# Performance work log

Hardware: AMD Instinct MI355X
Metric: run time of the kernel (lower is better)

The kernel has to match this reference:

```python
import jax, jax.numpy as jnp
import numpy as np

U = 356  # LSTM units

def _lstm(x, W, Wr, b, h0, c0):
    """Keras-style LSTM. x: [B,T,F]. Returns (hs [B,T,U], h [B,U], c [B,U])."""
    def step(carry, xt):
        h, c = carry
        z = xt @ W + h @ Wr + b            # [B, 4U], gate order i,f,g,o
        i, f, g, o = jnp.split(z, 4, axis=-1)
        c = jax.nn.sigmoid(f) * c + jax.nn.sigmoid(i) * jnp.tanh(g)
        h = jax.nn.sigmoid(o) * jnp.tanh(c)
        return (h, c), h
    (h, c), hs = jax.lax.scan(step, (h0, c0), jnp.swapaxes(x, 0, 1))
    return jnp.swapaxes(hs, 0, 1), h, c


def setup_inputs() -> dict:
    key = jax.random.key(0)
    ks = jax.random.split(key, 12)
    s = 0.05
    return {
        "x": jax.random.normal(ks[0], (8192, 7, 69), jnp.float32),
        "m": jax.random.normal(ks[1], (8192, 7, 45), jnp.float32),
        "enc_W": jax.random.normal(ks[2], (69, 4 * U), jnp.float32) * s,
        "enc_U": jax.random.normal(ks[3], (U, 4 * U), jnp.float32) * s,
        "enc_b": jnp.zeros((4 * U,), jnp.float32),
        "dec_W": jax.random.normal(ks[4], (45, 4 * U), jnp.float32) * s,
        "dec_U": jax.random.normal(ks[5], (U, 4 * U), jnp.float32) * s,
        "dec_b": jnp.zeros((4 * U,), jnp.float32),
        "W_map": jax.random.normal(ks[6], (7 * U, 1024), jnp.float32) * s,
        "b_map": jnp.zeros((1024,), jnp.float32),
        "W1": jax.random.normal(ks[7], (1024, 1024), jnp.float32) * s,
        "b1": jnp.zeros((1024,), jnp.float32),
        "W2": jax.random.normal(ks[8], (1024, 1024), jnp.float32) * s,
        "b2": jnp.zeros((1024,), jnp.float32),
        "W3": jax.random.normal(ks[9], (1024, 1024), jnp.float32) * s,
        "b3": jnp.zeros((1024,), jnp.float32),
        "W_out": jax.random.normal(ks[10], (1024, 168), jnp.float32) * s,
        "b_out": jnp.zeros((168,), jnp.float32),
    }


def reference(x, m, enc_W, enc_U, enc_b, dec_W, dec_U, dec_b,
              W_map, b_map, W1, b1, W2, b2, W3, b3, W_out, b_out):
    B = x.shape[0]
    h0 = jnp.zeros((B, U), x.dtype)
    c0 = jnp.zeros((B, U), x.dtype)
    # Encoder: only final states are used (dropout layers are identity at inference).
    _, s_h, s_c = _lstm(x, enc_W, enc_U, enc_b, h0, c0)
    # Decoder seeded with encoder states, returns full sequence [B,7,U].
    decoded, _, _ = _lstm(m, dec_W, dec_U, dec_b, s_h, s_c)
    f = decoded.reshape(B, -1)                     # [B, 7*356]
    h = jax.nn.relu(f @ W_map + b_map)
    h = jnp.tanh(h @ W1 + b1)
    h = jnp.tanh(h @ W2 + b2)
    h = jnp.tanh(h @ W3 + b3)
    return h @ W_out + b_out                        # [B, 168]
```

## Files before the change

kernel.cpp:

```cpp
#include <hip/hip_runtime.h>
#include <math.h>


using bf16x8 = __attribute__((ext_vector_type(8))) short;
using f32x4  = __attribute__((ext_vector_type(4))) float;

enum { EPI_NONE = 0, EPI_RELU = 1, EPI_TANH = 2 };

__device__ inline unsigned short f2bf(float f) {
    union { float f; unsigned u; } v; v.f = f;
    unsigned r = v.u + 0x7FFFu + ((v.u >> 16) & 1u);
    return (unsigned short)(r >> 16);
}
__device__ inline float sigf(float x) {
    return __fdividef(1.f, 1.f + __expf(-x));
}
__device__ inline float tanhfast(float x) {
    return 1.f - __fdividef(2.f, 1.f + __expf(2.f * x));
}

__device__ inline void gll16(const void* g, void* l) {
    __builtin_amdgcn_global_load_lds(
        (const __attribute__((address_space(1))) unsigned int*)(uintptr_t)g,
        (__attribute__((address_space(3))) unsigned int*)(unsigned int)(uintptr_t)l,
        16, 0, 0);
}

#define STAGE(A_, Bt_, K_, k0_, b_)                                            \
    {                                                                          \
        const int row = tid >> 2, kc = tid & 3;                                \
        gll16((A_)  + (size_t)(m0 + row) * (K_) + (k0_) + kc * 8,              \
              (void*)&As[b_][tid * 8]);                                        \
        gll16((Bt_) + (size_t)(n0 + row) * (K_) + (k0_) + kc * 8,              \
              (void*)&Bs[b_][tid * 8]);                                        \
    }

#define GEMM_CORE(A_, Bt_, K_)                                                 \
    STAGE(A_, Bt_, K_, 0, 0)                                                   \
    {                                                                          \
        const int niter = (K_) / 32;                                           \
        for (int it = 0; it < niter; ++it) {                                   \
            __syncthreads();                                                   \
            if (it + 1 < niter) {                                              \
                const int kn = (it + 1) * 32, bn = (it + 1) & 1;               \
                STAGE(A_, Bt_, K_, kn, bn)                                     \
            }                                                                  \
            const unsigned short* Asb = As[it & 1];                            \
            const unsigned short* Bsb = Bs[it & 1];                            \
            bf16x8 aF[2], bF[4];                                               \
            _Pragma("unroll")                                                  \
            for (int mi = 0; mi < 2; ++mi)                                     \
                aF[mi] = *(const bf16x8*)(Asb + (wr*32 + mi*16 + lm)*32 + quad*8);\
            _Pragma("unroll")                                                  \
            for (int ni = 0; ni < 4; ++ni)                                     \
                bF[ni] = *(const bf16x8*)(Bsb + (wc*64 + ni*16 + lm)*32 + quad*8);\
            _Pragma("unroll")                                                  \
            for (int mi = 0; mi < 2; ++mi)                                     \
                _Pragma("unroll")                                              \
                for (int ni = 0; ni < 4; ++ni)                                 \
                    acc[mi][ni] = __builtin_amdgcn_mfma_f32_16x16x32_bf16(     \
                        aF[mi], bF[ni], acc[mi][ni], 0, 0, 0);                 \
        }                                                                      \
    }

#define GEMM_PREAMBLE                                                          \
    __shared__ __attribute__((aligned(16))) unsigned short As[2][128 * 32];    \
    __shared__ __attribute__((aligned(16))) unsigned short Bs[2][128 * 32];    \
    const int tid  = threadIdx.x;                                              \
    const int lane = tid & 63;                                                 \
    const int w    = tid >> 6;                                       \
    const int wr   = w >> 1, wc = w & 1;                    \
    const int lm   = lane & 15, quad = lane >> 4;                              \
    const int m0   = blockIdx.x * 128, n0 = blockIdx.y * 128;                  \
    f32x4 acc[2][4] = {};

template <int EPI, int OUT_BF16, int NGUARD>
__global__ __launch_bounds__(512, 6)
void gemm_mfma(const unsigned short* __restrict__ A,
               const unsigned short* __restrict__ Bt,
               const float* __restrict__ bias,
               void* __restrict__ Cv, int ldc, int Nreal, int K)
{
    GEMM_PREAMBLE
    GEMM_CORE(A, Bt, K)
    #pragma unroll
    for (int mi = 0; mi < 2; ++mi)
        #pragma unroll
        for (int r = 0; r < 4; ++r) {
            const size_t row = m0 + wr * 32 + mi * 16 + quad * 4 + r;
            #pragma unroll
            for (int ni = 0; ni < 4; ++ni) {
                const int col = n0 + wc * 64 + ni * 16 + lm;
                if (!NGUARD || col < Nreal) {
                    float v = acc[mi][ni][r] + bias[col];
                    if (EPI == EPI_RELU) v = fmaxf(v, 0.f);
                    if (EPI == EPI_TANH) v = tanhfast(v);
                    if (OUT_BF16) ((unsigned short*)Cv)[row * ldc + col] = f2bf(v);
                    else          ((float*)Cv)[row * ldc + col] = v;
                }
            }
        }
}

__global__ __launch_bounds__(512, 6)
void gemm_lstm(const unsigned short* __restrict__ A,
               const unsigned short* __restrict__ Bt,
               const float* __restrict__ biasI,
               float* __restrict__ c,
               unsigned short* __restrict__ hdst, int ldh, int hoff,
               unsigned short* __restrict__ dec, int doff, int K)
{
    GEMM_PREAMBLE
    GEMM_CORE(A, Bt, K)
    const int u = ((n0 + wc * 64) >> 6) * 16 + lm;
    if (u >= 356) return;
    float bI[4];
    #pragma unroll
    for (int ni = 0; ni < 4; ++ni) bI[ni] = biasI[n0 + wc * 64 + ni * 16 + lm];
    #pragma unroll
    for (int mi = 0; mi < 2; ++mi)
        #pragma unroll
        for (int r = 0; r < 4; ++r) {
            const size_t row = m0 + wr * 32 + mi * 16 + quad * 4 + r;
            const float zi = acc[mi][0][r] + bI[0];
            const float zf = acc[mi][1][r] + bI[1];
            const float zg = acc[mi][2][r] + bI[2];
            const float zo = acc[mi][3][r] + bI[3];
            const size_t ci = row * 356 + u;
            const float cn = sigf(zf) * c[ci] + sigf(zi) * tanhfast(zg);
            c[ci] = cn;
            const unsigned short hb = f2bf(sigf(zo) * tanhfast(cn));
            if (hdst) hdst[row * (size_t)ldh + hoff + u] = hb;
            if (dec)  dec[row * (size_t)2496 + doff + u] = hb;
        }
}

struct PackArgs {
    const float *Wa0, *Wb0, *bias0; unsigned short* Wt0; float* bI0; int K10, K0, Kp0;
    const float *Wa1, *Wb1, *bias1; unsigned short* Wt1; float* bI1; int K11, K1, Kp1;
};
__global__ void pack_lstm2(PackArgs p)
{
    const float* Wa  = blockIdx.y ? p.Wa1  : p.Wa0;
    const float* Wb  = blockIdx.y ? p.Wb1  : p.Wb0;
    const float* bias= blockIdx.y ? p.bias1: p.bias0;
    unsigned short* Wt = blockIdx.y ? p.Wt1 : p.Wt0;
    float* biasI = blockIdx.y ? p.bI1 : p.bI0;
    const int K1 = blockIdx.y ? p.K11 : p.K10;
    const int K  = blockIdx.y ? p.K1  : p.K0;
    const int Kp = blockIdx.y ? p.Kp1 : p.Kp0;
    const int idx = blockIdx.x * 256 + threadIdx.x;
    if (idx >= 1536 * Kp) return;
    const int np = idx / Kp, k = idx - np * Kp;
    const int ub = np >> 6, g = (np >> 4) & 3, ul = np & 15;
    const int u = ub * 16 + ul;
    const bool valid = (u < 356);
    const int norig = g * 356 + u;
    float v = 0.f;
    if (valid && k < K)
        v = (k < K1) ? Wa[(size_t)k * 1424 + norig]
                     : Wb[(size_t)(k - K1) * 1424 + norig];
    Wt[(size_t)np * Kp + k] = f2bf(v);
    if (k == 0) biasI[np] = valid ? bias[norig] : 0.f;
}

__global__ void transpose_pack(const float* __restrict__ W, int K, int N,
                               unsigned short* __restrict__ Wt, int Kp, int Np)
{
    __shared__ float t[32][33];
    const int n0 = blockIdx.x * 32, k0 = blockIdx.y * 32;
    const int tx = threadIdx.x, ty = threadIdx.y;
    #pragma unroll
    for (int r = 0; r < 4; ++r) {
        const int k = k0 + ty + 8 * r, n = n0 + tx;
        t[ty + 8 * r][tx] = (k < K && n < N) ? W[(size_t)k * N + n] : 0.f;
    }
    __syncthreads();
    #pragma unroll
    for (int r = 0; r < 4; ++r) {
        const int k = k0 + tx, n = n0 + ty + 8 * r;
        if (k < Kp && n < Np) Wt[(size_t)n * Kp + k] = f2bf(t[tx][ty + 8 * r]);
    }
}

struct WP3 { const float *s0, *s1, *s2; unsigned short *d0, *d1, *d2; };
__global__ void transpose_pack3(WP3 p)
{
    __shared__ float t[32][33];
    const float* W = (blockIdx.z == 0) ? p.s0 : (blockIdx.z == 1) ? p.s1 : p.s2;
    unsigned short* Wt = (blockIdx.z == 0) ? p.d0 : (blockIdx.z == 1) ? p.d1 : p.d2;
    const int n0 = blockIdx.x * 32, k0 = blockIdx.y * 32;
    const int tx = threadIdx.x, ty = threadIdx.y;
    #pragma unroll
    for (int r = 0; r < 4; ++r)
        t[ty + 8 * r][tx] = W[(size_t)(k0 + ty + 8 * r) * 1024 + n0 + tx];
    __syncthreads();
    #pragma unroll
    for (int r = 0; r < 4; ++r)
        Wt[(size_t)(n0 + ty + 8 * r) * 1024 + k0 + tx] = f2bf(t[tx][ty + 8 * r]);
}

__global__ void zero_pads(unsigned short* __restrict__ AcE,
                          unsigned short* __restrict__ AcD,
                          unsigned short* __restrict__ dcd,
                          unsigned short* __restrict__ cc)
{
    const size_t N0 = (size_t)8192 * 379, N1 = (size_t)6 * 8192 * 23;
    const size_t N2 = (size_t)8192 * 371, N3 = (size_t)6 * 8192 * 15;
    const size_t N4 = (size_t)8192 * 4,   N5 = (size_t)8192 * 356 * 2;
    size_t i = (size_t)blockIdx.x * 256 + threadIdx.x;
    if (i < N0) { const size_t r = i / 379; AcE[r * 448 + 69 + i % 379] = 0; return; }
    i -= N0;
    if (i < N1) { const size_t r = 8192 + i / 23; AcE[r * 448 + 425 + i % 23] = 0; return; }
    i -= N1;
    if (i < N2) { const size_t r = i / 371; AcD[r * 416 + 45 + i % 371] = 0; return; }
    i -= N2;
    if (i < N3) { const size_t r = 8192 + i / 15; AcD[r * 416 + 401 + i % 15] = 0; return; }
    i -= N3;
    if (i < N4) { dcd[(i / 4) * 2496 + 2492 + (i & 3)] = 0; return; }
    i -= N4;
    if (i < N5) cc[i] = 0;
}

__global__ void fill_slices2(const float* __restrict__ x,
                             const float* __restrict__ m,
                             unsigned short* __restrict__ AcE,
                             unsigned short* __restrict__ AcD)
{
    const int NX = 8192 * 7 * 69;
    int i = blockIdx.x * 256 + threadIdx.x;
    if (i < NX) {
        const int b = i / (7 * 69), rem = i - b * 7 * 69;
        const int t = rem / 69, f = rem - t * 69;
        AcE[(size_t)t * 8192 * 448 + (size_t)b * 448 + f] = f2bf(x[i]);
        return;
    }
    i -= NX;
    if (i < 8192 * 7 * 45) {
        const int b = i / (7 * 45), rem = i - b * 7 * 45;
        const int t = rem / 45, f = rem - t * 45;
        AcD[(size_t)t * 8192 * 416 + (size_t)b * 416 + f] = f2bf(m[i]);
    }
}

extern "C" void kernel_launch(void* const* d_in, const int* in_sizes, int n_in,
                              void* d_out, int out_size, void* d_ws, size_t ws_size,
                              hipStream_t stream)
{
    const float* x     = (const float*)d_in[0];
    const float* m     = (const float*)d_in[1];
    const float* enc_W = (const float*)d_in[2];
    const float* enc_U = (const float*)d_in[3];
    const float* enc_b = (const float*)d_in[4];
    const float* dec_W = (const float*)d_in[5];
    const float* dec_Um= (const float*)d_in[6];
    const float* dec_b = (const float*)d_in[7];
    const float* W_map = (const float*)d_in[8];
    const float* b_map = (const float*)d_in[9];
    const float* W1    = (const float*)d_in[10];
    const float* b1    = (const float*)d_in[11];
    const float* W2    = (const float*)d_in[12];
    const float* b2    = (const float*)d_in[13];
    const float* W3    = (const float*)d_in[14];
    const float* b3    = (const float*)d_in[15];
    const float* W_out = (const float*)d_in[16];
    const float* b_out = (const float*)d_in[17];
    float* out = (float*)d_out;

    const int B = 8192, T = 7, FE = 69, FD = 45;
    const int KE = 448, KD = 416, KMP = 2496;

    char* ws = (char*)d_ws;
    size_t off = 0;
    auto alloc = [&](size_t bytes) -> void* {
        void* p = ws + off; off = (off + bytes + 255) & ~(size_t)255; return p;
    };
    unsigned short* WtE = (unsigned short*)alloc((size_t)1536 * KE * 2);
    unsigned short* WtD = (unsigned short*)alloc((size_t)1536 * KD * 2);
    unsigned short* WtM = (unsigned short*)alloc((size_t)1024 * KMP * 2);
    unsigned short* Wt1 = (unsigned short*)alloc((size_t)1024 * 1024 * 2);
    unsigned short* Wt2 = (unsigned short*)alloc((size_t)1024 * 1024 * 2);
    unsigned short* Wt3 = (unsigned short*)alloc((size_t)1024 * 1024 * 2);
    unsigned short* WtO = (unsigned short*)alloc((size_t)256 * 1024 * 2);
    float* bIE = (float*)alloc(1536 * 4);
    float* bID = (float*)alloc(1536 * 4);
    unsigned short* AcE = (unsigned short*)alloc((size_t)T * B * KE * 2);
    unsigned short* AcD = (unsigned short*)alloc((size_t)T * B * KD * 2);
    unsigned short* dcd = (unsigned short*)alloc((size_t)B * KMP * 2);
    unsigned short* a1  = (unsigned short*)alloc((size_t)B * 1024 * 2);
    unsigned short* a2  = (unsigned short*)alloc((size_t)B * 1024 * 2);
    float* c = (float*)alloc((size_t)B * 356 * 4);

    PackArgs pa{enc_W, enc_U, enc_b, WtE, bIE, FE, FE + 356, KE,
                dec_W, dec_Um, dec_b, WtD, bID, FD, FD + 356, KD};
    pack_lstm2<<<dim3((1536 * KE + 255) / 256, 2), 256, 0, stream>>>(pa);
    const dim3 tb(32, 8);
    transpose_pack<<<dim3(1024 / 32, KMP / 32), tb, 0, stream>>>(
        W_map, 2492, 1024, WtM, KMP, 1024);
    WP3 p3{W1, W2, W3, Wt1, Wt2, Wt3};
    transpose_pack3<<<dim3(32, 32, 3), tb, 0, stream>>>(p3);
    transpose_pack<<<dim3(256 / 32, 1024 / 32), tb, 0, stream>>>(
        W_out, 1024, 168, WtO, 1024, 256);

    {
        const size_t tot = (size_t)8192 * 379 + (size_t)6 * 8192 * 23
                         + (size_t)8192 * 371 + (size_t)6 * 8192 * 15
                         + (size_t)8192 * 4   + (size_t)8192 * 356 * 2;
        zero_pads<<<(unsigned)((tot + 255) / 256), 256, 0, stream>>>(
            AcE, AcD, dcd, (unsigned short*)c);
    }
    fill_slices2<<<(B * T * (FE + FD) + 255) / 256, 256, 0, stream>>>(
        x, m, AcE, AcD);

    const dim3 gz(64, 12);
    for (int t = 0; t < T; ++t) {
        unsigned short* At = AcE + (size_t)t * B * KE;
        unsigned short* hdst = (t < 6) ? AcE + (size_t)(t + 1) * B * KE : AcD;
        gemm_lstm<<<gz, 512, 0, stream>>>(
            At, WtE, bIE, c, hdst, (t < 6) ? KE : KD, (t < 6) ? FE : FD,
            nullptr, 0, KE);
    }
    for (int t = 0; t < T; ++t) {
        unsigned short* At = AcD + (size_t)t * B * KD;
        unsigned short* hdst = (t < 6) ? AcD + (size_t)(t + 1) * B * KD : nullptr;
        gemm_lstm<<<gz, 512, 0, stream>>>(
            At, WtD, bID, c, hdst, KD, FD, dcd, t * 356, KD);
    }

    gemm_mfma<EPI_RELU, 1, 0><<<dim3(64, 8), 512, 0, stream>>>(
        dcd, WtM, b_map, a1, 1024, 1024, KMP);
    gemm_mfma<EPI_TANH, 1, 0><<<dim3(64, 8), 512, 0, stream>>>(
        a1, Wt1, b1, a2, 1024, 1024, 1024);
    gemm_mfma<EPI_TANH, 1, 0><<<dim3(64, 8), 512, 0, stream>>>(
        a2, Wt2, b2, a1, 1024, 1024, 1024);
    gemm_mfma<EPI_TANH, 1, 0><<<dim3(64, 8), 512, 0, stream>>>(
        a1, Wt3, b3, a2, 1024, 1024, 1024);
    gemm_mfma<EPI_NONE, 0, 1><<<dim3(64, 2), 512, 0, stream>>>(
        a2, WtO, b_out, out, 168, 168, 1024);
}
```

Before: 614.3 us.

## Fuse all 14 LSTM timesteps into one persistent kernel with on-chip state

Replaces the 14 per-timestep GEMM+cell launches, the padding-zero kernel and the input-slice fill kernel with a single persistent kernel. Each block owns 32 batch rows, keeps h in LDS and c in registers across all encoder and decoder steps, and converts x/m into LDS on the fly. Weights are streamed from global/L2 directly into registers each step. This removes launch overhead and the global round-trips for h, c and the staged inputs. In exchange, only 256 blocks run, each repeatedly rereading the full weight matrix without LDS staging, which may limit MFMA utilisation.

```diff
diff --git a/kernel.cpp b/kernel.cpp
--- a/kernel.cpp
+++ b/kernel.cpp
@@ -25,6 +25,121 @@
         (__attribute__((address_space(3))) unsigned int*)(unsigned int)(uintptr_t)l,
         16, 0, 0);
 }
+
+#define PROWS 32
+#define PLDA  456
+
+__global__ __launch_bounds__(512, 2)
+void lstm_persist(const float* __restrict__ x,
+                  const float* __restrict__ m,
+                  const unsigned short* __restrict__ WtE,
+                  const unsigned short* __restrict__ WtD,
+                  const float* __restrict__ bIE,
+                  const float* __restrict__ bID,
+                  unsigned short* __restrict__ dcd)
+{
+    __shared__ __attribute__((aligned(16))) unsigned short Ab[PROWS * PLDA];
+    const int tid  = threadIdx.x;
+    const int lane = tid & 63;
+    const int w    = tid >> 6;
+    const int lm   = lane & 15, quad = lane >> 4;
+    const int brow = blockIdx.x * PROWS;
+
+    for (int i = tid; i < PROWS * PLDA; i += 512) Ab[i] = 0;
+    __syncthreads();
+    for (int i = tid; i < PROWS * 69; i += 512) {
+        const int r = i / 69, f = i - r * 69;
+        Ab[r * PLDA + f] = f2bf(x[((size_t)(brow + r) * 7 + 0) * 69 + f]);
+    }
+
+    float creg[2][3][4] = {};
+    float bI[3][4];
+
+    for (int s = 0; s < 14; ++s) {
+        const bool enc = (s < 7);
+        const int t = enc ? s : s - 7;
+        const unsigned short* Wt = enc ? WtE : WtD;
+        const unsigned short* wbase =
+            Wt + (size_t)(w * 192 + lm) * 448 + quad * 8;
+
+        if (s == 0 || s == 7) {
+            const float* bsrc = enc ? bIE : bID;
+            #pragma unroll
+            for (int a = 0; a < 3; ++a)
+                #pragma unroll
+                for (int g = 0; g < 4; ++g)
+                    bI[a][g] = bsrc[(3 * w + a) * 64 + g * 16 + lm];
+        }
+
+        __syncthreads();
+
+        f32x4 acc[2][12] = {};
+        #pragma unroll 2
+        for (int kk = 0; kk < 14; ++kk) {
+            bf16x8 aF[2];
+            #pragma unroll
+            for (int mi = 0; mi < 2; ++mi)
+                aF[mi] = *(const bf16x8*)&Ab[(mi * 16 + lm) * PLDA
+                                             + kk * 32 + quad * 8];
+            bf16x8 bF[12];
+            #pragma unroll
+            for (int ni = 0; ni < 12; ++ni)
+                bF[ni] = *(const bf16x8*)(wbase + (size_t)ni * 16 * 448
+                                          + kk * 32);
+            #pragma unroll
+            for (int ni = 0; ni < 12; ++ni) {
+                acc[0][ni] = __builtin_amdgcn_mfma_f32_16x16x32_bf16(
+                    aF[0], bF[ni], acc[0][ni], 0, 0, 0);
+                acc[1][ni] = __builtin_amdgcn_mfma_f32_16x16x32_bf16(
+                    aF[1], bF[ni], acc[1][ni], 0, 0, 0);
+            }
+        }
+
+        __syncthreads();
+
+        const int hoff = (s < 6) ? 69 : 45;
+        #pragma unroll
+        for (int mi = 0; mi < 2; ++mi)
+            #pragma unroll
+            for (int a = 0; a < 3; ++a) {
+                const int u = (3 * w + a) * 16 + lm;
+                const bool uok = (u < 356);
+                #pragma unroll
+                for (int r = 0; r < 4; ++r) {
+                    const float zi = acc[mi][a * 4 + 0][r] + bI[a][0];
+                    const float zf = acc[mi][a * 4 + 1][r] + bI[a][1];
+                    const float zg = acc[mi][a * 4 + 2][r] + bI[a][2];
+                    const float zo = acc[mi][a * 4 + 3][r] + bI[a][3];
+                    const float cn = sigf(zf) * creg[mi][a][r]
+                                   + sigf(zi) * tanhfast(zg);
+                    creg[mi][a][r] = cn;
+                    const unsigned short hb = f2bf(sigf(zo) * tanhfast(cn));
+                    const int rl = mi * 16 + quad * 4 + r;
+                    if (uok) {
+                        if (s < 13) Ab[rl * PLDA + hoff + u] = hb;
+                        if (!enc)
+                            dcd[(size_t)(brow + rl) * 2496 + t * 356 + u] = hb;
+                    }
+                }
+            }
+
+        const int sn = s + 1;
+        if (sn < 7) {
+            for (int i = tid; i < PROWS * 69; i += 512) {
+                const int r = i / 69, f = i - r * 69;
+                Ab[r * PLDA + f] =
+                    f2bf(x[((size_t)(brow + r) * 7 + sn) * 69 + f]);
+            }
+        } else if (sn < 14) {
+            for (int i = tid; i < PROWS * 45; i += 512) {
+                const int r = i / 45, f = i - r * 45;
+                Ab[r * PLDA + f] =
+                    f2bf(m[((size_t)(brow + r) * 7 + (sn - 7)) * 45 + f]);
+            }
+        }
+    }
+}
+
 
 #define STAGE(A_, Bt_, K_, k0_, b_)                                            \
     {                                                                          \
@@ -102,39 +217,6 @@
         }
 }
 
-__global__ __launch_bounds__(512, 6)
-void gemm_lstm(const unsigned short* __restrict__ A,
-               const unsigned short* __restrict__ Bt,
-               const float* __restrict__ biasI,
-               float* __restrict__ c,
-               unsigned short* __restrict__ hdst, int ldh, int hoff,
-               unsigned short* __restrict__ dec, int doff, int K)
-{
-    GEMM_PREAMBLE
-    GEMM_CORE(A, Bt, K)
-    const int u = ((n0 + wc * 64) >> 6) * 16 + lm;
-    if (u >= 356) return;
-    float bI[4];
-    #pragma unroll
-    for (int ni = 0; ni < 4; ++ni) bI[ni] = biasI[n0 + wc * 64 + ni * 16 + lm];
-    #pragma unroll
-    for (int mi = 0; mi < 2; ++mi)
-        #pragma unroll
-        for (int r = 0; r < 4; ++r) {
-            const size_t row = m0 + wr * 32 + mi * 16 + quad * 4 + r;
-            const float zi = acc[mi][0][r] + bI[0];
-            const float zf = acc[mi][1][r] + bI[1];
-            const float zg = acc[mi][2][r] + bI[2];
-            const float zo = acc[mi][3][r] + bI[3];
-            const size_t ci = row * 356 + u;
-            const float cn = sigf(zf) * c[ci] + sigf(zi) * tanhfast(zg);
-            c[ci] = cn;
-            const unsigned short hb = f2bf(sigf(zo) * tanhfast(cn));
-            if (hdst) hdst[row * (size_t)ldh + hoff + u] = hb;
-            if (dec)  dec[row * (size_t)2496 + doff + u] = hb;
-        }
-}
-
 struct PackArgs {
     const float *Wa0, *Wb0, *bias0; unsigned short* Wt0; float* bI0; int K10, K0, Kp0;
     const float *Wa1, *Wb1, *bias1; unsigned short* Wt1; float* bI1; int K11, K1, Kp1;
@@ -200,47 +282,10 @@
         Wt[(size_t)(n0 + ty + 8 * r) * 1024 + k0 + tx] = f2bf(t[tx][ty + 8 * r]);
 }
 
-__global__ void zero_pads(unsigned short* __restrict__ AcE,
-                          unsigned short* __restrict__ AcD,
-                          unsigned short* __restrict__ dcd,
-                          unsigned short* __restrict__ cc)
-{
-    const size_t N0 = (size_t)8192 * 379, N1 = (size_t)6 * 8192 * 23;
-    const size_t N2 = (size_t)8192 * 371, N3 = (size_t)6 * 8192 * 15;
-    const size_t N4 = (size_t)8192 * 4,   N5 = (size_t)8192 * 356 * 2;
-    size_t i = (size_t)blockIdx.x * 256 + threadIdx.x;
-    if (i < N0) { const size_t r = i / 379; AcE[r * 448 + 69 + i % 379] = 0; return; }
-    i -= N0;
-    if (i < N1) { const size_t r = 8192 + i / 23; AcE[r * 448 + 425 + i % 23] = 0; return; }
-    i -= N1;
-    if (i < N2) { const size_t r = i / 371; AcD[r * 416 + 45 + i % 371] = 0; return; }
-    i -= N2;
-    if (i < N3) { const size_t r = 8192 + i / 15; AcD[r * 416 + 401 + i % 15] = 0; return; }
-    i -= N3;
-    if (i < N4) { dcd[(i / 4) * 2496 + 2492 + (i & 3)] = 0; return; }
-    i -= N4;
-    if (i < N5) cc[i] = 0;
-}
-
-__global__ void fill_slices2(const float* __restrict__ x,
-                             const float* __restrict__ m,
-                             unsigned short* __restrict__ AcE,
-                             unsigned short* __restrict__ AcD)
-{
-    const int NX = 8192 * 7 * 69;
-    int i = blockIdx.x * 256 + threadIdx.x;
-    if (i < NX) {
-        const int b = i / (7 * 69), rem = i - b * 7 * 69;
-        const int t = rem / 69, f = rem - t * 69;
-        AcE[(size_t)t * 8192 * 448 + (size_t)b * 448 + f] = f2bf(x[i]);
-        return;
-    }
-    i -= NX;
-    if (i < 8192 * 7 * 45) {
-        const int b = i / (7 * 45), rem = i - b * 7 * 45;
-        const int t = rem / 45, f = rem - t * 45;
-        AcD[(size_t)t * 8192 * 416 + (size_t)b * 416 + f] = f2bf(m[i]);
-    }
+__global__ void zero_dcd_pad(unsigned short* __restrict__ dcd)
+{
+    const int i = blockIdx.x * 256 + threadIdx.x;
+    if (i < 8192 * 4) dcd[(size_t)(i >> 2) * 2496 + 2492 + (i & 3)] = 0;
 }
 
 extern "C" void kernel_launch(void* const* d_in, const int* in_sizes, int n_in,
@@ -267,16 +312,16 @@
     const float* b_out = (const float*)d_in[17];
     float* out = (float*)d_out;
 
-    const int B = 8192, T = 7, FE = 69, FD = 45;
-    const int KE = 448, KD = 416, KMP = 2496;
+    const int B = 8192, FE = 69, FD = 45;
+    const int KMP = 2496;
 
     char* ws = (char*)d_ws;
     size_t off = 0;
     auto alloc = [&](size_t bytes) -> void* {
         void* p = ws + off; off = (off + bytes + 255) & ~(size_t)255; return p;
     };
-    unsigned short* WtE = (unsigned short*)alloc((size_t)1536 * KE * 2);
-    unsigned short* WtD = (unsigned short*)alloc((size_t)1536 * KD * 2);
+    unsigned short* WtE = (unsigned short*)alloc((size_t)1536 * 448 * 2);
+    unsigned short* WtD = (unsigned short*)alloc((size_t)1536 * 448 * 2);
     unsigned short* WtM = (unsigned short*)alloc((size_t)1024 * KMP * 2);
     unsigned short* Wt1 = (unsigned short*)alloc((size_t)1024 * 1024 * 2);
     unsigned short* Wt2 = (unsigned short*)alloc((size_t)1024 * 1024 * 2);
@@ -284,16 +329,13 @@
     unsigned short* WtO = (unsigned short*)alloc((size_t)256 * 1024 * 2);
     float* bIE = (float*)alloc(1536 * 4);
     float* bID = (float*)alloc(1536 * 4);
-    unsigned short* AcE = (unsigned short*)alloc((size_t)T * B * KE * 2);
-    unsigned short* AcD = (unsigned short*)alloc((size_t)T * B * KD * 2);
     unsigned short* dcd = (unsigned short*)alloc((size_t)B * KMP * 2);
     unsigned short* a1  = (unsigned short*)alloc((size_t)B * 1024 * 2);
     unsigned short* a2  = (unsigned short*)alloc((size_t)B * 1024 * 2);
-    float* c = (float*)alloc((size_t)B * 356 * 4);
-
-    PackArgs pa{enc_W, enc_U, enc_b, WtE, bIE, FE, FE + 356, KE,
-                dec_W, dec_Um, dec_b, WtD, bID, FD, FD + 356, KD};
-    pack_lstm2<<<dim3((1536 * KE + 255) / 256, 2), 256, 0, stream>>>(pa);
+
+    PackArgs pa{enc_W, enc_U, enc_b, WtE, bIE, FE, FE + 356, 448,
+                dec_W, dec_Um, dec_b, WtD, bID, FD, FD + 356, 448};
+    pack_lstm2<<<dim3((1536 * 448 + 255) / 256, 2), 256, 0, stream>>>(pa);
     const dim3 tb(32, 8);
     transpose_pack<<<dim3(1024 / 32, KMP / 32), tb, 0, stream>>>(
         W_map, 2492, 1024, WtM, KMP, 1024);
@@ -301,31 +343,9 @@
     transpose_pack3<<<dim3(32, 32, 3), tb, 0, stream>>>(p3);
     transpose_pack<<<dim3(256 / 32, 1024 / 32), tb, 0, stream>>>(
         W_out, 1024, 168, WtO, 1024, 256);
-
-    {
-        const size_t tot = (size_t)8192 * 379 + (size_t)6 * 8192 * 23
-                         + (size_t)8192 * 371 + (size_t)6 * 8192 * 15
-                         + (size_t)8192 * 4   + (size_t)8192 * 356 * 2;
-        zero_pads<<<(unsigned)((tot + 255) / 256), 256, 0, stream>>>(
-            AcE, AcD, dcd, (unsigned short*)c);
-    }
-    fill_slices2<<<(B * T * (FE + FD) + 255) / 256, 256, 0, stream>>>(
-        x, m, AcE, AcD);
-
-    const dim3 gz(64, 12);
-    for (int t = 0; t < T; ++t) {
-        unsigned short* At = AcE + (size_t)t * B * KE;
-        unsigned short* hdst = (t < 6) ? AcE + (size_t)(t + 1) * B * KE : AcD;
-        gemm_lstm<<<gz, 512, 0, stream>>>(
-            At, WtE, bIE, c, hdst, (t < 6) ? KE : KD, (t < 6) ? FE : FD,
-            nullptr, 0, KE);
-    }
-    for (int t = 0; t < T; ++t) {
-        unsigned short* At = AcD + (size_t)t * B * KD;
-        unsigned short* hdst = (t < 6) ? AcD + (size_t)(t + 1) * B * KD : nullptr;
-        gemm_lstm<<<gz, 512, 0, stream>>>(
-            At, WtD, bID, c, hdst, KD, FD, dcd, t * 356, KD);
-    }
+    zero_dcd_pad<<<(8192 * 4 + 255) / 256, 256, 0, stream>>>(dcd);
+
+    lstm_persist<<<256, 512, 0, stream>>>(x, m, WtE, WtD, bIE, bID, dcd);
 
     gemm_mfma<EPI_RELU, 1, 0><<<dim3(64, 8), 512, 0, stream>>>(
         dcd, WtM, b_map, a1, 1024, 1024, KMP);
```

Result: slower. 917.8 us (+49.4%).
